# Performance work log

Measured on AMD Instinct MI355X. Metric: run time of the kernel, lower is better.

## Reference

```python
import jax, jax.numpy as jnp
import numpy as np
from jax import lax

EPS = 1e-5

def _conv(x, w, pad):
    return lax.conv_general_dilated(
        x, w, window_strides=(1, 1), padding=[(pad, pad), (pad, pad)],
        dimension_numbers=('NCHW', 'OIHW', 'NCHW'))

def _bn(x, p):
    # p: [4, C] rows = gamma, beta, running_mean, running_var (inference BN)
    g, b, m, v = p[0], p[1], p[2], p[3]
    scale = g / jnp.sqrt(v + EPS)
    return x * scale[None, :, None, None] + (b - m * scale)[None, :, None, None]

def _cbr(x, w, p, relu=True):
    y = _bn(_conv(x, w, pad=1), p)
    return jax.nn.relu(y) if relu else y

def _make_bn(key, c):
    k1, k2, k3 = jax.random.split(key, 3)
    gamma = jnp.ones((c,), jnp.float32) + 0.05 * jax.random.normal(k1, (c,))
    beta = 0.1 * jax.random.normal(k2, (c,))
    mean = 0.1 * jax.random.normal(k3, (c,))
    var = jax.random.uniform(k1, (c,), minval=0.5, maxval=1.5)
    return jnp.stack([gamma, beta, mean, var]).astype(jnp.float32)

def setup_inputs() -> dict:
    key = jax.random.key(0)
    ks = jax.random.split(key, 12)
    C, M = 256, 64  # channels, bottleneck width (hard-coded 64 in source)
    B, H, W = 8, 128, 128
    s = lambda fan: 1.0 / np.sqrt(fan)
    return {
        'x': jax.random.normal(ks[0], (B, C, H, W), jnp.float32),
        'w_res': jax.random.normal(ks[1], (C, C, 1, 1), jnp.float32) * s(C),
        'bn_res': _make_bn(ks[2], C),
        'w_vpre': jax.random.normal(ks[3], (M, C, 3, 3), jnp.float32) * s(C * 9),
        'bn_vpre': _make_bn(ks[4], M),
        'w_hpre': jax.random.normal(ks[5], (M, C, 3, 3), jnp.float32) * s(C * 9),
        'bn_hpre': _make_bn(ks[6], M),
        'w_add': jax.random.normal(ks[7], (C, M, 3, 3), jnp.float32) * s(M * 9),
        'bn_add': _make_bn(ks[8], C),
        'w_post': jax.random.normal(ks[9], (C, C, 3, 3), jnp.float32) * s(C * 9),
        'bn_post': _make_bn(ks[10], C),
    }

def reference(x, w_res, bn_res, w_vpre, bn_vpre, w_hpre, bn_hpre,
              w_add, bn_add, w_post, bn_post):
    # residual branch: 1x1 conv + BN (no relu)
    res = _bn(_conv(x, w_res, pad=0), bn_res)
    # vertical branch: conv-bn-relu then TopPool (reverse cumulative max over H)
    p1 = _cbr(x, w_vpre, bn_vpre)
    pool1 = lax.cummax(p1, axis=2, reverse=True)
    # horizontal branch: conv-bn-relu then LeftPool (reverse cumulative max over W)
    p2 = _cbr(x, w_hpre, bn_hpre)
    pool2 = lax.cummax(p2, axis=3, reverse=True)
    # merge: conv-bn (no relu), residual add, relu, post conv-bn-relu
    merged = _cbr(pool1 + pool2, w_add, bn_add, relu=False)
    out = jax.nn.relu(res + merged)
    return _cbr(out, w_post, bn_post)
```

## Files before the change

kernel.cpp:

```cpp
#include <hip/hip_runtime.h>
#include <hip/hip_bf16.h>


using bf16x8  = __attribute__((ext_vector_type(8))) __bf16;
using floatx4 = __attribute__((ext_vector_type(4))) float;

typedef __attribute__((address_space(1))) const uint32_t gas_u32;
typedef __attribute__((address_space(3))) uint32_t las_u32;

__device__ __forceinline__ float bf2f(__hip_bfloat16 h) { return __bfloat162float(h); }
__device__ __forceinline__ __hip_bfloat16 f2bf(float f) { return __float2bfloat16(f); }


__global__ __launch_bounds__(256) void k_cast_x(const float* __restrict__ x,
                                                __hip_bfloat16* __restrict__ xb) {
    __shared__ float t[64][65];
    const int n  = blockIdx.z;
    const int h  = blockIdx.y;
    const int c0 = (blockIdx.x >> 1) * 64;
    const int w0 = (blockIdx.x & 1) * 64;
    const int tid = threadIdx.x;
#pragma unroll
    for (int it = 0; it < 16; ++it) {
        int idx = it * 256 + tid;
        int c = idx >> 6, w = idx & 63;
        t[c][w] = x[(((size_t)n * 256 + c0 + c) * 128 + h) * 128 + w0 + w];
    }
    __syncthreads();
#pragma unroll
    for (int it = 0; it < 16; ++it) {
        int idx = it * 256 + tid;
        int w = idx >> 6, c = idx & 63;
        xb[(((size_t)n * 128 + h) * 128 + w0 + w) * 256 + c0 + c] = f2bf(t[c][w]);
    }
}

__global__ void k_prep_bn(const float* __restrict__ p, float* __restrict__ sc,
                          float* __restrict__ bi, int C) {
    int i = blockIdx.x * 64 + threadIdx.x;
    if (i >= C) return;
    float g = p[i], b = p[C + i], m = p[2 * C + i], v = p[3 * C + i];
    float s = g / sqrtf(v + 1e-5f);
    sc[i] = s;
    bi[i] = b - m * s;
}

__global__ void k_reorder_w3(const float* __restrict__ src, __hip_bfloat16* __restrict__ dst,
                             const float* __restrict__ scale, int Cin, int CoutTot,
                             int co_off, int total) {
    int i = blockIdx.x * 256 + threadIdx.x;
    if (i >= total) return;
    int ci  = i % Cin;
    int tap = (i / Cin) % 9;
    int co  = i / (Cin * 9);
    dst[((((size_t)tap * (Cin >> 5) + (ci >> 5)) * CoutTot) + co_off + co) * 32 + (ci & 31)] =
        f2bf(src[((size_t)co * Cin + ci) * 9 + tap] * scale[co]);
}

__global__ void k_reorder_w1(const float* __restrict__ src, __hip_bfloat16* __restrict__ dst,
                             const float* __restrict__ scale, int Cin, int total) {
    int i = blockIdx.x * 256 + threadIdx.x;
    if (i >= total) return;
    dst[i] = f2bf(src[i] * scale[i / Cin]);
}


__global__ __launch_bounds__(256) void k_pool1(__hip_bfloat16* __restrict__ b) {
    const int idx = blockIdx.x * 256 + threadIdx.x;
    const int c = idx & 63;
    const int w = (idx >> 6) & 127;
    const int n = idx >> 13;
    const size_t stride = 128 * 64;
    const size_t base = ((size_t)n * 128 * 128 + w) * 64 + c;
    float m = 0.0f;
    for (int hb = 31; hb >= 0; --hb) {
        size_t a0 = base + (size_t)(4 * hb) * stride;
        float v0 = bf2f(b[a0]);
        float v1 = bf2f(b[a0 + stride]);
        float v2 = bf2f(b[a0 + 2 * stride]);
        float v3 = bf2f(b[a0 + 3 * stride]);
        float m3 = fmaxf(m, v3);
        float m2 = fmaxf(m3, v2);
        float m1 = fmaxf(m2, v1);
        float m0 = fmaxf(m1, v0);
        b[a0 + 3 * stride] = f2bf(m3);
        b[a0 + 2 * stride] = f2bf(m2);
        b[a0 + stride]     = f2bf(m1);
        b[a0]              = f2bf(m0);
        m = m0;
    }
}

__global__ __launch_bounds__(256) void k_pool2(__hip_bfloat16* __restrict__ b,
                                               const __hip_bfloat16* __restrict__ pl) {
    const int idx = blockIdx.x * 256 + threadIdx.x;
    const int c = idx & 63;
    const int h = (idx >> 6) & 127;
    const int n = idx >> 13;
    const size_t base = (((size_t)n * 128 + h) * 128) * 64 + c;
    float m = 0.0f;
    for (int wb = 31; wb >= 0; --wb) {
        size_t a0 = base + (size_t)(4 * wb) * 64;
        float v0 = bf2f(b[a0]);
        float v1 = bf2f(b[a0 + 64]);
        float v2 = bf2f(b[a0 + 128]);
        float v3 = bf2f(b[a0 + 192]);
        float u0 = bf2f(pl[a0]);
        float u1 = bf2f(pl[a0 + 64]);
        float u2 = bf2f(pl[a0 + 128]);
        float u3 = bf2f(pl[a0 + 192]);
        float m3 = fmaxf(m, v3);
        float m2 = fmaxf(m3, v2);
        float m1 = fmaxf(m2, v1);
        float m0 = fmaxf(m1, v0);
        b[a0 + 192] = f2bf(m3 + u3);
        b[a0 + 128] = f2bf(m2 + u2);
        b[a0 + 64]  = f2bf(m1 + u1);
        b[a0]       = f2bf(m0 + u0);
        m = m0;
    }
}

__global__ __launch_bounds__(256) void conv1x1(const __hip_bfloat16* __restrict__ xin,
                                               const __hip_bfloat16* __restrict__ wgt,
                                               const float* __restrict__ bias,
                                               __hip_bfloat16* __restrict__ out) {
    __shared__ __align__(16) __hip_bfloat16 Xs[128 * 64];
    __shared__ __align__(16) __hip_bfloat16 Ws[128 * 64];
    const int tid  = threadIdx.x;
    const int lane = tid & 63;
    const int wid  = tid >> 6;
    const int wm = wid >> 1, wn = wid & 1;
    const int p0 = blockIdx.x * 128;
    const int c0 = blockIdx.y * 128;
    const int q = lane >> 4, r16 = lane & 15;

    floatx4 acc[4][4] = {};

    for (int k0 = 0; k0 < 256; k0 += 64) {
#pragma unroll
        for (int it = 0; it < 4; ++it) {
            const int pp = it * 32 + (tid >> 3);
            const int g  = tid & 7;
            uint4 val = *(const uint4*)(xin + ((size_t)(p0 + pp) * 256 + k0 + g * 8));
            *(uint4*)(&Xs[pp * 64 + (((g + pp) & 7) * 8)]) = val;
        }
#pragma unroll
        for (int it = 0; it < 4; ++it) {
            const int rr = it * 32 + (tid >> 3);
            const int g  = tid & 7;
            uint4 val = *(const uint4*)(wgt + ((size_t)(c0 + rr) * 256 + k0 + g * 8));
            *(uint4*)(&Ws[rr * 64 + (((g + rr) & 7) * 8)]) = val;
        }
        __syncthreads();
#pragma unroll
        for (int ks = 0; ks < 2; ++ks) {
            bf16x8 afr[4], bfr[4];
#pragma unroll
            for (int i = 0; i < 4; ++i) {
                const int pp = wm * 64 + i * 16 + r16;
                const int g  = ks * 4 + q;
                afr[i] = *(const bf16x8*)(&Xs[pp * 64 + (((g + pp) & 7) * 8)]);
            }
#pragma unroll
            for (int j = 0; j < 4; ++j) {
                const int rr = wn * 64 + j * 16 + r16;
                const int g  = ks * 4 + q;
                bfr[j] = *(const bf16x8*)(&Ws[rr * 64 + (((g + rr) & 7) * 8)]);
            }
#pragma unroll
            for (int i = 0; i < 4; ++i)
#pragma unroll
                for (int j = 0; j < 4; ++j)
                    acc[i][j] = __builtin_amdgcn_mfma_f32_16x16x32_bf16(afr[i], bfr[j], acc[i][j], 0, 0, 0);
        }
        __syncthreads();
    }
#pragma unroll
    for (int j = 0; j < 4; ++j) {
        const int co = c0 + wn * 64 + j * 16 + r16;
        const float bi = bias[co];
#pragma unroll
        for (int i = 0; i < 4; ++i) {
            const int pb = p0 + wm * 64 + i * 16 + q * 4;
#pragma unroll
            for (int r = 0; r < 4; ++r)
                out[(size_t)(pb + r) * 256 + co] = f2bf(acc[i][j][r] + bi);
        }
    }
}

template <int CIN, int COUT, int MODE>
__global__ __launch_bounds__(512, 2) void conv3x3(const __hip_bfloat16* __restrict__ xin,
                                                  const __hip_bfloat16* __restrict__ wgt,
                                                  const float* __restrict__ bias,
                                                  void* __restrict__ out,
                                                  const __hip_bfloat16* __restrict__ resbuf,
                                                  __hip_bfloat16* __restrict__ out2) {
    constexpr int NCH = CIN / 32;
    constexpr int NPH = 3 * NCH;
    __shared__ __align__(16) __hip_bfloat16 Xs[2][6 * 130 * 32];
    __shared__ __align__(16) __hip_bfloat16 Ws[2][3 * 128 * 32];
    const int tid  = threadIdx.x;
    const int lane = tid & 63;
    const int wid  = tid >> 6;
    const int wm   = wid >> 1;
    const int wn   = wid & 1;
    const int bx   = blockIdx.x;
    const int n     = bx >> 5;
    const int hbase = (bx & 31) * 4;
    const int co_off = blockIdx.y * 128;
    const int q = lane >> 4, r16 = lane & 15;

    const int le = lane >> 2, lp = lane & 3;
    const int xe = wid * 16 + 1 + le;
    const int xg = (lp - ((xe >> 1) & 3)) & 3;
    const int xlaneoff = (xe - 1) * CIN + xg * 8;
    const int wrow = wid * 16 + le;
    const int wg2 = (lp - ((wrow >> 1) & 3)) & 3;
    const int wlaneoff = wrow * 32 + wg2 * 8;

    floatx4 acc[4][2][4] = {};

    auto stageX = [&](int c) {
        const int ci0 = c * 32;
        __hip_bfloat16* xbuf = Xs[c & 1];
#pragma unroll
        for (int r = 0; r < 6; ++r) {
            const int hh = hbase - 1 + r;
            if (0 <= hh && hh < 128) {
                const __hip_bfloat16* src =
                    xin + ((size_t)(n * 128 + hh) * 128) * CIN + ci0 + xlaneoff;
                __builtin_amdgcn_global_load_lds((gas_u32*)src,
                    (las_u32*)&xbuf[((size_t)r * 130 + wid * 16 + 1) * 32], 16, 0, 0);
            } else {
                *(uint4*)(&xbuf[((size_t)r * 130 + xe) * 32 + lp * 8]) =
                    make_uint4(0u, 0u, 0u, 0u);
            }
        }
    };
    auto stageW = [&](int ph) {
        const int t0 = (ph % 3) * 3;
        const int c  = ph / 3;
        __hip_bfloat16* wbuf = Ws[ph & 1];
#pragma unroll
        for (int t = 0; t < 3; ++t) {
            const __hip_bfloat16* src =
                wgt + ((size_t)((t0 + t) * NCH + c) * COUT + co_off) * 32 + wlaneoff;
            __builtin_amdgcn_global_load_lds((gas_u32*)src,
                (las_u32*)&wbuf[((size_t)t * 128 + wid * 16) * 32], 16, 0, 0);
        }
    };

    if (tid < 96) {
        int b = tid / 48, rem = tid % 48;
        int r = rem >> 3, side = (rem >> 2) & 1, p = rem & 3;
        *(uint4*)(&Xs[b][((size_t)r * 130 + (side ? 129 : 0)) * 32 + p * 8]) =
            make_uint4(0u, 0u, 0u, 0u);
    }
    stageX(0);
    stageW(0);
    __syncthreads();

    for (int c = 0; c < NCH; ++c) {
#pragma unroll
        for (int k = 0; k < 3; ++k) {
            const int p = 3 * c + k;
            if (p + 1 < NPH) stageW(p + 1);
            if (k == 0 && c + 1 < NCH) stageX(c + 1);
            __builtin_amdgcn_sched_barrier(0);
            const __hip_bfloat16* xbuf = Xs[c & 1];
            const __hip_bfloat16* wbuf = Ws[p & 1];
#pragma unroll
            for (int t = 0; t < 3; ++t) {
                const int dw = t - 1;
                bf16x8 bfr[4];
#pragma unroll
                for (int j = 0; j < 4; ++j) {
                    const int row = wn * 64 + j * 16 + r16;
                    const int pg  = (q + ((row >> 1) & 3)) & 3;
                    bfr[j] = *(const bf16x8*)(&wbuf[((size_t)t * 128 + row) * 32 + pg * 8]);
                }
#pragma unroll
                for (int row = 0; row < 4; ++row) {
                    bf16x8 afr[2];
#pragma unroll
                    for (int i = 0; i < 2; ++i) {
                        const int e  = wm * 32 + i * 16 + r16 + dw + 1;
                        const int pg = (q + ((e >> 1) & 3)) & 3;
                        afr[i] = *(const bf16x8*)(&xbuf[((size_t)(row + k) * 130 + e) * 32 + pg * 8]);
                    }
#pragma unroll
                    for (int i = 0; i < 2; ++i)
#pragma unroll
                        for (int j = 0; j < 4; ++j) {
                            if (MODE == 3)
                                acc[row][i][j] = __builtin_amdgcn_mfma_f32_16x16x32_bf16(bfr[j], afr[i], acc[row][i][j], 0, 0, 0);
                            else
                                acc[row][i][j] = __builtin_amdgcn_mfma_f32_16x16x32_bf16(afr[i], bfr[j], acc[row][i][j], 0, 0, 0);
                        }
                }
            }
            __syncthreads();
        }
    }

    if (MODE == 1) {
#pragma unroll
        for (int row = 0; row < 4; ++row) {
            const int h = hbase + row;
#pragma unroll
            for (int j = 0; j < 4; ++j) {
                const int co = wn * 64 + j * 16 + r16;
                const float bi = bias[co];
                __hip_bfloat16* ob = (co < 64) ? (__hip_bfloat16*)out : out2;
                const int ch = co & 63;
#pragma unroll
                for (int i = 0; i < 2; ++i) {
#pragma unroll
                    for (int r = 0; r < 4; ++r) {
                        const int w = wm * 32 + i * 16 + q * 4 + r;
                        const size_t p = (size_t)(n * 128 + h) * 128 + w;
                        ob[p * 64 + ch] = f2bf(fmaxf(acc[row][i][j][r] + bi, 0.0f));
                    }
                }
            }
        }
    } else if (MODE == 2) {
        __hip_bfloat16* o = (__hip_bfloat16*)out;
#pragma unroll
        for (int row = 0; row < 4; ++row) {
            const int h = hbase + row;
#pragma unroll
            for (int j = 0; j < 4; ++j) {
                const int co = co_off + wn * 64 + j * 16 + r16;
                const float bi = bias[co];
#pragma unroll
                for (int i = 0; i < 2; ++i) {
#pragma unroll
                    for (int r = 0; r < 4; ++r) {
                        const int w = wm * 32 + i * 16 + q * 4 + r;
                        const size_t p = (size_t)(n * 128 + h) * 128 + w;
                        float v = acc[row][i][j][r] + bi + bf2f(resbuf[p * 256 + co]);
                        o[p * 256 + co] = f2bf(fmaxf(v, 0.0f));
                    }
                }
            }
        }
    } else {
        float* o = (float*)out;
#pragma unroll
        for (int row = 0; row < 4; ++row) {
            const int h = hbase + row;
#pragma unroll
            for (int j = 0; j < 4; ++j) {
#pragma unroll
                for (int r = 0; r < 4; ++r) {
                    const int co = co_off + wn * 64 + j * 16 + q * 4 + r;
                    const float bi = bias[co];
#pragma unroll
                    for (int i = 0; i < 2; ++i) {
                        const int w = wm * 32 + i * 16 + r16;
                        float v = fmaxf(acc[row][i][j][r] + bi, 0.0f);
                        o[(((size_t)(n * 256 + co)) * 128 + h) * 128 + w] = v;
                    }
                }
            }
        }
    }
}


extern "C" void kernel_launch(void* const* d_in, const int* in_sizes, int n_in,
                              void* d_out, int out_size, void* d_ws, size_t ws_size,
                              hipStream_t stream) {
    const float* x       = (const float*)d_in[0];
    const float* w_res   = (const float*)d_in[1];
    const float* bn_res  = (const float*)d_in[2];
    const float* w_vpre  = (const float*)d_in[3];
    const float* bn_vpre = (const float*)d_in[4];
    const float* w_hpre  = (const float*)d_in[5];
    const float* bn_hpre = (const float*)d_in[6];
    const float* w_add   = (const float*)d_in[7];
    const float* bn_add  = (const float*)d_in[8];
    const float* w_post  = (const float*)d_in[9];
    const float* bn_post = (const float*)d_in[10];

    const size_t SZ_XB = (size_t)8 * 128 * 128 * 256 * 2;
    const size_t SZ_P  = (size_t)8 * 128 * 128 * 64 * 2;

    char* w = (char*)d_ws;
    __hip_bfloat16* xb   = (__hip_bfloat16*)(w);
    __hip_bfloat16* resb = (__hip_bfloat16*)(w + SZ_XB);
    __hip_bfloat16* p1   = (__hip_bfloat16*)(w + 2 * SZ_XB);
    __hip_bfloat16* p2   = (__hip_bfloat16*)(w + 2 * SZ_XB + SZ_P);
    char* wp = w + 2 * SZ_XB + 2 * SZ_P;
    __hip_bfloat16* wres  = (__hip_bfloat16*)wp; wp += (size_t)65536 * 2;
    __hip_bfloat16* wpre  = (__hip_bfloat16*)wp; wp += (size_t)9 * 128 * 256 * 2;
    __hip_bfloat16* wadd  = (__hip_bfloat16*)wp; wp += (size_t)9 * 256 * 64 * 2;
    __hip_bfloat16* wpost = (__hip_bfloat16*)wp; wp += (size_t)9 * 256 * 256 * 2;
    float* sc_res  = (float*)wp; wp += 256 * 4;
    float* bi_res  = (float*)wp; wp += 256 * 4;
    float* sc_pre  = (float*)wp; wp += 128 * 4;
    float* bi_pre  = (float*)wp; wp += 128 * 4;
    float* sc_add  = (float*)wp; wp += 256 * 4;
    float* bi_add  = (float*)wp; wp += 256 * 4;
    float* sc_post = (float*)wp; wp += 256 * 4;
    float* bi_post = (float*)wp; wp += 256 * 4;

    k_prep_bn<<<4, 64, 0, stream>>>(bn_res, sc_res, bi_res, 256);
    k_prep_bn<<<1, 64, 0, stream>>>(bn_vpre, sc_pre, bi_pre, 64);
    k_prep_bn<<<1, 64, 0, stream>>>(bn_hpre, sc_pre + 64, bi_pre + 64, 64);
    k_prep_bn<<<4, 64, 0, stream>>>(bn_add, sc_add, bi_add, 256);
    k_prep_bn<<<4, 64, 0, stream>>>(bn_post, sc_post, bi_post, 256);

    k_reorder_w1<<<256, 256, 0, stream>>>(w_res, wres, sc_res, 256, 65536);
    k_reorder_w3<<<576, 256, 0, stream>>>(w_vpre, wpre, sc_pre, 256, 128, 0, 147456);
    k_reorder_w3<<<576, 256, 0, stream>>>(w_hpre, wpre, sc_pre + 64, 256, 128, 64, 147456);
    k_reorder_w3<<<576, 256, 0, stream>>>(w_add, wadd, sc_add, 64, 256, 0, 147456);
    k_reorder_w3<<<2304, 256, 0, stream>>>(w_post, wpost, sc_post, 256, 256, 0, 589824);

    k_cast_x<<<dim3(8, 128, 8), 256, 0, stream>>>(x, xb);

    conv1x1<<<dim3(1024, 2), 256, 0, stream>>>(xb, wres, bi_res, resb);
    conv3x3<256, 128, 1><<<dim3(256, 1), 512, 0, stream>>>(xb, wpre, bi_pre, p1, nullptr, p2);
    k_pool1<<<256, 256, 0, stream>>>(p1);
    k_pool2<<<256, 256, 0, stream>>>(p2, p1);
    conv3x3<64, 256, 2><<<dim3(256, 2), 512, 0, stream>>>(p2, wadd, bi_add, xb, resb, nullptr);
    conv3x3<256, 256, 3><<<dim3(256, 2), 512, 0, stream>>>(xb, wpost, bi_post, d_out, nullptr, nullptr);
}
```

Before: 417.0 us.

## Pipeline 3x3 conv weights per tap with 4-slot ring and fine-grained vmcnt waits

Replaces the two-buffer, three-tap-per-phase weight staging with a four-slot ring that holds one tap's weights per slot and prefetches three taps ahead. The main loop is unrolled into nine per-tap phases. Each phase waits with an explicit s_waitcnt vmcnt count and s_barrier instead of a full __syncthreads, so global->LDS loads stay in flight across taps. The goal is to hide weight and input load latency behind MFMA work and to cut barrier stalls, at the cost of more barriers per channel chunk and hand-tuned vmcnt counts that must match the exact number of outstanding loads.

```diff
diff --git a/kernel.cpp b/kernel.cpp
--- a/kernel.cpp
+++ b/kernel.cpp
@@ -198,9 +198,8 @@
                                                   const __hip_bfloat16* __restrict__ resbuf,
                                                   __hip_bfloat16* __restrict__ out2) {
     constexpr int NCH = CIN / 32;
-    constexpr int NPH = 3 * NCH;
     __shared__ __align__(16) __hip_bfloat16 Xs[2][6 * 130 * 32];
-    __shared__ __align__(16) __hip_bfloat16 Ws[2][3 * 128 * 32];
+    __shared__ __align__(16) __hip_bfloat16 Ws[4][128 * 32];
     const int tid  = threadIdx.x;
     const int lane = tid & 63;
     const int wid  = tid >> 6;
@@ -239,16 +238,39 @@
             }
         }
     };
-    auto stageW = [&](int ph) {
-        const int t0 = (ph % 3) * 3;
-        const int c  = ph / 3;
-        __hip_bfloat16* wbuf = Ws[ph & 1];
-#pragma unroll
-        for (int t = 0; t < 3; ++t) {
-            const __hip_bfloat16* src =
-                wgt + ((size_t)((t0 + t) * NCH + c) * COUT + co_off) * 32 + wlaneoff;
-            __builtin_amdgcn_global_load_lds((gas_u32*)src,
-                (las_u32*)&wbuf[((size_t)t * 128 + wid * 16) * 32], 16, 0, 0);
+    auto stageW = [&](int cc, int tap, int slot) {
+        const __hip_bfloat16* src =
+            wgt + ((size_t)(tap * NCH + cc) * COUT + co_off) * 32 + wlaneoff;
+        __builtin_amdgcn_global_load_lds((gas_u32*)src,
+            (las_u32*)&Ws[slot][wid * 16 * 32], 16, 0, 0);
+    };
+    auto taps = [&](int tap, const __hip_bfloat16* wbuf, const __hip_bfloat16* xbuf) {
+        const int tr = tap / 3, dw = tap % 3 - 1;
+        bf16x8 bfr[4];
+#pragma unroll
+        for (int j = 0; j < 4; ++j) {
+            const int row = wn * 64 + j * 16 + r16;
+            const int pg  = (q + ((row >> 1) & 3)) & 3;
+            bfr[j] = *(const bf16x8*)(&wbuf[(size_t)row * 32 + pg * 8]);
+        }
+#pragma unroll
+        for (int row = 0; row < 4; ++row) {
+            bf16x8 afr[2];
+#pragma unroll
+            for (int i = 0; i < 2; ++i) {
+                const int e  = wm * 32 + i * 16 + r16 + dw + 1;
+                const int pg = (q + ((e >> 1) & 3)) & 3;
+                afr[i] = *(const bf16x8*)(&xbuf[((size_t)(row + tr) * 130 + e) * 32 + pg * 8]);
+            }
+#pragma unroll
+            for (int i = 0; i < 2; ++i)
+#pragma unroll
+                for (int j = 0; j < 4; ++j) {
+                    if (MODE == 3)
+                        acc[row][i][j] = __builtin_amdgcn_mfma_f32_16x16x32_bf16(bfr[j], afr[i], acc[row][i][j], 0, 0, 0);
+                    else
+                        acc[row][i][j] = __builtin_amdgcn_mfma_f32_16x16x32_bf16(afr[i], bfr[j], acc[row][i][j], 0, 0, 0);
+                }
         }
     };
 
@@ -258,52 +280,51 @@
         *(uint4*)(&Xs[b][((size_t)r * 130 + (side ? 129 : 0)) * 32 + p * 8]) =
             make_uint4(0u, 0u, 0u, 0u);
     }
+    stageW(0, 0, 0);
+    stageW(0, 1, 1);
+    stageW(0, 2, 2);
     stageX(0);
-    stageW(0);
     __syncthreads();
 
-    for (int c = 0; c < NCH; ++c) {
-#pragma unroll
-        for (int k = 0; k < 3; ++k) {
-            const int p = 3 * c + k;
-            if (p + 1 < NPH) stageW(p + 1);
-            if (k == 0 && c + 1 < NCH) stageX(c + 1);
-            __builtin_amdgcn_sched_barrier(0);
-            const __hip_bfloat16* xbuf = Xs[c & 1];
-            const __hip_bfloat16* wbuf = Ws[p & 1];
-#pragma unroll
-            for (int t = 0; t < 3; ++t) {
-                const int dw = t - 1;
-                bf16x8 bfr[4];
-#pragma unroll
-                for (int j = 0; j < 4; ++j) {
-                    const int row = wn * 64 + j * 16 + r16;
-                    const int pg  = (q + ((row >> 1) & 3)) & 3;
-                    bfr[j] = *(const bf16x8*)(&wbuf[((size_t)t * 128 + row) * 32 + pg * 8]);
-                }
-#pragma unroll
-                for (int row = 0; row < 4; ++row) {
-                    bf16x8 afr[2];
-#pragma unroll
-                    for (int i = 0; i < 2; ++i) {
-                        const int e  = wm * 32 + i * 16 + r16 + dw + 1;
-                        const int pg = (q + ((e >> 1) & 3)) & 3;
-                        afr[i] = *(const bf16x8*)(&xbuf[((size_t)(row + k) * 130 + e) * 32 + pg * 8]);
-                    }
-#pragma unroll
-                    for (int i = 0; i < 2; ++i)
-#pragma unroll
-                        for (int j = 0; j < 4; ++j) {
-                            if (MODE == 3)
-                                acc[row][i][j] = __builtin_amdgcn_mfma_f32_16x16x32_bf16(bfr[j], afr[i], acc[row][i][j], 0, 0, 0);
-                            else
-                                acc[row][i][j] = __builtin_amdgcn_mfma_f32_16x16x32_bf16(afr[i], bfr[j], acc[row][i][j], 0, 0, 0);
-                        }
-                }
-            }
-            __syncthreads();
-        }
-    }
+#define CP_VMCNT(N) asm volatile("s_waitcnt vmcnt(" #N ")" ::: "memory")
+#define CP_PHASE(T, WISS, XISS, VM) do {                                      \
+        if (WISS) stageW(c + (((T) + 3) / 9), ((T) + 3) % 9,                  \
+                         (c + (T) + 3) & 3);                                  \
+        __builtin_amdgcn_sched_barrier(0);                                    \
+        if (XISS) stageX(c + 1);                                              \
+        __builtin_amdgcn_sched_barrier(0);                                    \
+        taps((T), &Ws[(c + (T)) & 3][0], xbuf);                               \
+        CP_VMCNT(VM);                                                         \
+        __builtin_amdgcn_s_barrier();                                         \
+    } while (0)
+
+    for (int c = 0; c < NCH - 1; ++c) {
+        const __hip_bfloat16* xbuf = Xs[c & 1];
+        CP_PHASE(0, true, true,  8);
+        CP_PHASE(1, true, false, 8);
+        CP_PHASE(2, true, false, 2);
+        CP_PHASE(3, true, false, 2);
+        CP_PHASE(4, true, false, 2);
+        CP_PHASE(5, true, false, 2);
+        CP_PHASE(6, true, false, 2);
+        CP_PHASE(7, true, false, 2);
+        CP_PHASE(8, true, false, 2);
+    }
+    {
+        const int c = NCH - 1;
+        const __hip_bfloat16* xbuf = Xs[c & 1];
+        CP_PHASE(0, true, false, 2);
+        CP_PHASE(1, true, false, 2);
+        CP_PHASE(2, true, false, 2);
+        CP_PHASE(3, true, false, 2);
+        CP_PHASE(4, true, false, 2);
+        CP_PHASE(5, true, false, 2);
+        CP_PHASE(6, false, false, 1);
+        CP_PHASE(7, false, false, 0);
+        taps(8, &Ws[(c + 8) & 3][0], xbuf);
+    }
+#undef CP_PHASE
+#undef CP_VMCNT
 
     if (MODE == 1) {
 #pragma unroll
```

Result: slower. 427.3 us (+2.5%).
